# Optimization experiments

Measured on AMD Instinct MI355X. Metric: run time of the kernel, lower is better.

Reference implementation:

```python
import jax, jax.numpy as jnp
import numpy as np

N, E, FN, FE, L, G = 4096, 16384, 16, 8, 128, 64
EPS = 1e-5


def setup_inputs() -> dict:
    key = jax.random.key(0)
    ks = iter(jax.random.split(key, 40))

    def lin_w(shape):
        return jax.random.normal(next(ks), shape, jnp.float32) * (1.0 / np.sqrt(shape[0]))

    d = {}
    d["x"] = jax.random.normal(next(ks), (N, FN), jnp.float32)
    d["edge_attr"] = jax.random.normal(next(ks), (E, FE), jnp.float32)
    d["edge_index"] = jax.random.randint(next(ks), (2, E), 0, N)
    d["batch"] = jnp.sort(jax.random.randint(next(ks), (N,), 0, G))
    for i, (cin, cout) in enumerate([(FN, 32), (32, 64), (64, 128)], 1):
        d[f"We{i}"] = lin_w((FE, cin * cout))          # edge_fc weight
        d[f"be{i}"] = jnp.zeros((cin * cout,), jnp.float32)
        d[f"bias{i}"] = jnp.zeros((cout,), jnp.float32)
        d[f"Wr{i}"] = lin_w((cin, cout))               # res_fc weight
        d[f"br{i}"] = jnp.zeros((cout,), jnp.float32)
        d[f"bn_g{i}"] = jnp.ones((cout,), jnp.float32)
        d[f"bn_b{i}"] = jnp.zeros((cout,), jnp.float32)
        d[f"a{i}"] = jnp.float32(0.25)                  # PReLU slope
    d["Wi"] = lin_w((128, 128)); d["bi"] = jnp.zeros((128,), jnp.float32)
    d["Wj"] = lin_w((128, 128)); d["bj"] = jnp.zeros((128,), jnp.float32)
    d["Wfc"] = lin_w((128, 2 * L)); d["bfc"] = jnp.zeros((2 * L,), jnp.float32)
    return d


def _ecc(x, src, dst, norm, edge_attr, We, be, bias, Wr, br, cout, cin):
    # dynamically generated per-edge filter: [E, out, in]
    theta = (edge_attr @ We + be).reshape(E, cout, cin)
    # gather source features, per-edge matvec, degree-normalize (norm_j)
    msg = norm[src][:, None] * jnp.einsum('eoi,ei->eo', theta, x[src])
    # scatter-add into destination nodes + bias + residual linear
    return jax.ops.segment_sum(msg, dst, num_segments=N) + bias + x @ Wr + br


def _bn(x, g, b):
    m = x.mean(0)
    v = x.var(0)  # biased variance, as torch BN training normalization
    return (x - m) * jax.lax.rsqrt(v + EPS) * g + b


def _prelu(x, a):
    return jnp.where(x >= 0, x, a * x)


def reference(x, edge_attr, edge_index, batch,
              We1, be1, bias1, Wr1, br1, bn_g1, bn_b1, a1,
              We2, be2, bias2, Wr2, br2, bn_g2, bn_b2, a2,
              We3, be3, bias3, Wr3, br3, bn_g3, bn_b3, a3,
              Wi, bi, Wj, bj, Wfc, bfc):
    src, dst = edge_index[0], edge_index[1]
    deg = jax.ops.segment_sum(jnp.ones((E,), x.dtype), src, num_segments=N)
    norm = jnp.where(deg > 0, 1.0 / deg, 0.0)

    h = _ecc(x, src, dst, norm, edge_attr, We1, be1, bias1, Wr1, br1, 32, FN)
    h = _prelu(_bn(h, bn_g1, bn_b1), a1)
    h = _ecc(h, src, dst, norm, edge_attr, We2, be2, bias2, Wr2, br2, 64, 32)
    h = _prelu(_bn(h, bn_g2, bn_b2), a2)
    h = _ecc(h, src, dst, norm, edge_attr, We3, be3, bias3, Wr3, br3, 128, 64)
    h = _prelu(_bn(h, bn_g3, bn_b3), a3)

    # gated attention pooling (GGS-NN eq. 7), scatter-sum per graph
    gates = jax.nn.sigmoid(h @ Wi + bi)
    feats = jnp.tanh(h @ Wj + bj)
    pooled = jnp.tanh(jax.ops.segment_sum(gates * feats, batch, num_segments=G))

    z = pooled @ Wfc + bfc  # [G, 2L]
    return z[:, :L], z[:, L:]
```

## Files before the change

kernel.cpp:

```cpp
#include <hip/hip_runtime.h>
#include <math.h>

#define NN 4096
#define NE 16384
#define NG 64

#define OFF_DEG   0
#define OFF_H1    4096
#define OFF_H2    135168
#define OFF_H3    397312
#define OFF_ST1   921600
#define OFF_ST2   921664
#define OFF_ST3   921792
#define OFF_POOL  922048
#define OFF_WC1   930240
#define OFF_WC2   934848
#define OFF_WC3   953280
#define OFF_Y     1027008
#define ZERO_FLOATS 930240

__device__ __forceinline__ void tr_wcat(const float* We, const float* be,
                                        float* Wcat, int CIN, int COUT, int t) {
    int nine = 9 * COUT;
    int i = t / nine; int r = t - i * nine;
    int f = r / COUT; int o = r - f * COUT;
    Wcat[t] = (f < 8) ? We[f * CIN * COUT + o * CIN + i] : be[o * CIN + i];
}

__global__ __launch_bounds__(256) void k_prep(
    const float* __restrict__ We1, const float* __restrict__ be1,
    const float* __restrict__ We2, const float* __restrict__ be2,
    const float* __restrict__ We3, const float* __restrict__ be3,
    const int* __restrict__ ei, float* __restrict__ ws)
{
    int t = blockIdx.x * 256 + threadIdx.x;
    if (t < 4608)  { tr_wcat(We1, be1, ws + OFF_WC1, 16, 32, t); return; }
    t -= 4608;
    if (t < 18432) { tr_wcat(We2, be2, ws + OFF_WC2, 32, 64, t); return; }
    t -= 18432;
    if (t < 73728) { tr_wcat(We3, be3, ws + OFF_WC3, 64, 128, t); return; }
    t -= 73728;
    if (t < NE)    { atomicAdd(&ws[OFF_DEG + ei[t]], 1.0f); }
}

template<int K, bool BN>
__global__ __launch_bounds__(256) void k_proj(
    const float* __restrict__ A, const float* __restrict__ Bm,
    const float* __restrict__ deg, float* __restrict__ Y, int Ncols,
    const float* __restrict__ st, const float* __restrict__ g,
    const float* __restrict__ b, const float* __restrict__ a)
{
    __shared__ float sA[K][68];
    __shared__ float sB[K][68];
    __shared__ float sS[K];
    __shared__ float sT[K];
    const int tid = threadIdx.x;
    const int m0 = blockIdx.x * 64;
    const int n0 = blockIdx.y * 64;

    float al = 0.f;
    if constexpr (BN) {
        if (tid < K) {
            float mean = st[tid] * (1.f / NN);
            float var  = st[K + tid] * (1.f / NN) - mean * mean;
            var = fmaxf(var, 0.f);
            float s = rsqrtf(var + 1e-5f) * g[tid];
            sS[tid] = s;
            sT[tid] = b[tid] - mean * s;
        }
        al = a[0];
        __syncthreads();
    }

    for (int t = tid; t < 64 * K; t += 256) {
        int m = t / K, i = t - m * K;
        float v = A[(m0 + m) * K + i];
        if constexpr (BN) {
            v = fmaf(v, sS[i], sT[i]);
            v = v >= 0.f ? v : al * v;
        }
        sA[i][m] = v;
    }
    for (int t = tid; t < 64 * K; t += 256) {
        int i = t >> 6, n = t & 63;
        int col = n0 + n;
        sB[i][n] = (col < Ncols) ? Bm[i * Ncols + col] : 0.f;
    }
    __syncthreads();

    const int tn = tid & 15, tm = tid >> 4;
    float acc[4][4] = {{0.f}};
#pragma unroll 8
    for (int i = 0; i < K; ++i) {
        float4 av = *(const float4*)&sA[i][tm * 4];
        float4 bv = *(const float4*)&sB[i][tn * 4];
        acc[0][0] += av.x * bv.x; acc[0][1] += av.x * bv.y; acc[0][2] += av.x * bv.z; acc[0][3] += av.x * bv.w;
        acc[1][0] += av.y * bv.x; acc[1][1] += av.y * bv.y; acc[1][2] += av.y * bv.z; acc[1][3] += av.y * bv.w;
        acc[2][0] += av.z * bv.x; acc[2][1] += av.z * bv.y; acc[2][2] += av.z * bv.z; acc[2][3] += av.z * bv.w;
        acc[3][0] += av.w * bv.x; acc[3][1] += av.w * bv.y; acc[3][2] += av.w * bv.z; acc[3][3] += av.w * bv.w;
    }

#pragma unroll
    for (int mm = 0; mm < 4; ++mm) {
        int m = m0 + tm * 4 + mm;
        float d = deg[m];
        float nrm = d > 0.f ? 1.f / d : 0.f;
#pragma unroll
        for (int nn = 0; nn < 4; ++nn) {
            int col = n0 + tn * 4 + nn;
            if (col < Ncols) Y[(size_t)m * Ncols + col] = acc[mm][nn] * nrm;
        }
    }
}

template<int COUT>
__global__ __launch_bounds__(256) void k_egather(
    const float* __restrict__ Y, const float* __restrict__ eattr,
    const int* __restrict__ ei, float* __restrict__ h)
{
    int idx = blockIdx.x * 256 + threadIdx.x;
    int e = idx / COUT;
    int o = idx - e * COUT;
    int src = ei[e], dst = ei[NE + e];
    const float* y = Y + (size_t)src * (9 * COUT);
    const float* ea = eattr + e * 8;
    float acc = y[8 * COUT + o];
#pragma unroll
    for (int f = 0; f < 8; ++f) acc += ea[f] * y[f * COUT + o];
    atomicAdd(&h[dst * COUT + o], acc);
}

template<int CIN, int COUT, int KN, bool BN>
__global__ __launch_bounds__(256) void k_node(
    const float* __restrict__ xin, const float* __restrict__ Wr,
    const float* __restrict__ br, const float* __restrict__ bias,
    float* __restrict__ h, float* __restrict__ st_out,
    const float* __restrict__ st_in, const float* __restrict__ g,
    const float* __restrict__ b, const float* __restrict__ a)
{
    constexpr int NL = 256 / COUT;
    constexpr int NB = NL * KN;
    constexpr int CINP = CIN | 1;
    __shared__ float sWr[CIN * COUT];
    __shared__ float sX[NB * CINP];
    __shared__ float sred[256];
    __shared__ float sS[CIN];
    __shared__ float sT[CIN];
    const int tid = threadIdx.x;
    const int nbase = blockIdx.x * NB;

    if constexpr (BN) {
        if (tid < CIN) {
            float mean = st_in[tid] * (1.f / NN);
            float var  = st_in[CIN + tid] * (1.f / NN) - mean * mean;
            var = fmaxf(var, 0.f);
            float s = rsqrtf(var + 1e-5f) * g[tid];
            sS[tid] = s;
            sT[tid] = b[tid] - mean * s;
        }
    }
    for (int t = tid; t < CIN * COUT; t += 256) sWr[t] = Wr[t];
    __syncthreads();
    float al = 0.f;
    if constexpr (BN) al = a[0];

    for (int t = tid; t < NB * CIN; t += 256) {
        int r = t / CIN, i = t - r * CIN;
        float v = xin[(nbase + r) * CIN + i];
        if constexpr (BN) {
            v = fmaf(v, sS[i], sT[i]);
            v = v >= 0.f ? v : al * v;
        }
        sX[r * CINP + i] = v;
    }
    __syncthreads();

    const int o = tid % COUT;
    const int nl = tid / COUT;
    const float addc = bias[o] + br[o];
    float sum = 0.f, sumsq = 0.f;
#pragma unroll
    for (int k = 0; k < KN; ++k) {
        int r = nl * KN + k;
        float acc = addc;
        for (int i = 0; i < CIN; ++i)
            acc += sX[r * CINP + i] * sWr[i * COUT + o];
        int gi = (nbase + r) * COUT + o;
        float hv = h[gi] + acc;
        h[gi] = hv;
        sum += hv; sumsq += hv * hv;
    }
    sred[tid] = sum;
    __syncthreads();
    if (tid < COUT) {
        float s = 0.f;
        for (int q = 0; q < NL; ++q) s += sred[q * COUT + tid];
        atomicAdd(&st_out[tid], s);
    }
    __syncthreads();
    sred[tid] = sumsq;
    __syncthreads();
    if (tid < COUT) {
        float s = 0.f;
        for (int q = 0; q < NL; ++q) s += sred[q * COUT + tid];
        atomicAdd(&st_out[COUT + tid], s);
    }
}

__global__ __launch_bounds__(256) void k_pool(
    const float* __restrict__ h3, const int* __restrict__ batch,
    const float* __restrict__ Wi, const float* __restrict__ bi,
    const float* __restrict__ Wj, const float* __restrict__ bj,
    float* __restrict__ pooled,
    const float* __restrict__ st, const float* __restrict__ g,
    const float* __restrict__ b, const float* __restrict__ a)
{
    constexpr int KN = 8, NB = 16;
    __shared__ float sH[NB * 128];
    __shared__ int sB[NB];
    __shared__ float sS[128];
    __shared__ float sT[128];
    const int tid = threadIdx.x;
    const int nbase = blockIdx.x * NB;

    if (tid < 128) {
        float mean = st[tid] * (1.f / NN);
        float var  = st[128 + tid] * (1.f / NN) - mean * mean;
        var = fmaxf(var, 0.f);
        float s = rsqrtf(var + 1e-5f) * g[tid];
        sS[tid] = s;
        sT[tid] = b[tid] - mean * s;
    }
    if (tid < NB) sB[tid] = batch[nbase + tid];
    __syncthreads();
    const float al = a[0];

    for (int t = tid; t < NB * 128; t += 256) {
        int c = t & 127;
        float v = h3[nbase * 128 + t];
        v = fmaf(v, sS[c], sT[c]);
        v = v >= 0.f ? v : al * v;
        sH[t] = v;
    }
    __syncthreads();

    const int o = tid & 127, nl = tid >> 7;
    float gacc[KN], facc[KN];
#pragma unroll
    for (int k = 0; k < KN; ++k) { gacc[k] = 0.f; facc[k] = 0.f; }
    for (int i = 0; i < 128; ++i) {
        float wi = Wi[i * 128 + o], wj = Wj[i * 128 + o];
#pragma unroll
        for (int k = 0; k < KN; ++k) {
            float hv = sH[(nl * KN + k) * 128 + i];
            gacc[k] += hv * wi;
            facc[k] += hv * wj;
        }
    }
    float bio = bi[o], bjo = bj[o];
    float psum = 0.f;
    int curg = sB[nl * KN];
#pragma unroll
    for (int k = 0; k < KN; ++k) {
        int r = nl * KN + k;
        int bg = sB[r];
        if (bg != curg) {
            atomicAdd(&pooled[curg * 128 + o], psum);
            psum = 0.f; curg = bg;
        }
        float gate = 1.f / (1.f + expf(-(gacc[k] + bio)));
        float feat = tanhf(facc[k] + bjo);
        psum += gate * feat;
    }
    atomicAdd(&pooled[curg * 128 + o], psum);
}

__global__ __launch_bounds__(256) void k_final(
    const float* __restrict__ pooled, const float* __restrict__ Wfc,
    const float* __restrict__ bfc, float* __restrict__ out)
{
    __shared__ float sP[128];
    const int g = blockIdx.x, c = threadIdx.x;
    if (c < 128) sP[c] = tanhf(pooled[g * 128 + c]);
    __syncthreads();
    float z = bfc[c];
    for (int i = 0; i < 128; ++i) z += sP[i] * Wfc[i * 256 + c];
    int oidx = (c < 128) ? (g * 128 + c) : (NG * 128 + g * 128 + (c - 128));
    out[oidx] = z;
}

extern "C" void kernel_launch(void* const* d_in, const int* in_sizes, int n_in,
                              void* d_out, int out_size, void* d_ws, size_t ws_size,
                              hipStream_t stream)
{
    (void)in_sizes; (void)n_in; (void)out_size; (void)ws_size;
    const float* x     = (const float*)d_in[0];
    const float* eattr = (const float*)d_in[1];
    const int*   ei    = (const int*)d_in[2];
    const int*   batch = (const int*)d_in[3];
    const float* We1 = (const float*)d_in[4];
    const float* be1 = (const float*)d_in[5];
    const float* bias1 = (const float*)d_in[6];
    const float* Wr1 = (const float*)d_in[7];
    const float* br1 = (const float*)d_in[8];
    const float* bg1 = (const float*)d_in[9];
    const float* bb1 = (const float*)d_in[10];
    const float* a1  = (const float*)d_in[11];
    const float* We2 = (const float*)d_in[12];
    const float* be2 = (const float*)d_in[13];
    const float* bias2 = (const float*)d_in[14];
    const float* Wr2 = (const float*)d_in[15];
    const float* br2 = (const float*)d_in[16];
    const float* bg2 = (const float*)d_in[17];
    const float* bb2 = (const float*)d_in[18];
    const float* a2  = (const float*)d_in[19];
    const float* We3 = (const float*)d_in[20];
    const float* be3 = (const float*)d_in[21];
    const float* bias3 = (const float*)d_in[22];
    const float* Wr3 = (const float*)d_in[23];
    const float* br3 = (const float*)d_in[24];
    const float* bg3 = (const float*)d_in[25];
    const float* bb3 = (const float*)d_in[26];
    const float* a3  = (const float*)d_in[27];
    const float* Wi  = (const float*)d_in[28];
    const float* bi  = (const float*)d_in[29];
    const float* Wj  = (const float*)d_in[30];
    const float* bj  = (const float*)d_in[31];
    const float* Wfc = (const float*)d_in[32];
    const float* bfc = (const float*)d_in[33];
    float* ws  = (float*)d_ws;
    float* out = (float*)d_out;

    hipMemsetAsync(d_ws, 0, (size_t)ZERO_FLOATS * sizeof(float), stream);
    k_prep<<<442, 256, 0, stream>>>(We1, be1, We2, be2, We3, be3, ei, ws);

    k_proj<16, false><<<dim3(64, 5), 256, 0, stream>>>(
        x, ws + OFF_WC1, ws + OFF_DEG, ws + OFF_Y, 288,
        nullptr, nullptr, nullptr, nullptr);
    k_egather<32><<<NE * 32 / 256, 256, 0, stream>>>(ws + OFF_Y, eattr, ei, ws + OFF_H1);
    k_node<16, 32, 2, false><<<NN / 16, 256, 0, stream>>>(
        x, Wr1, br1, bias1, ws + OFF_H1, ws + OFF_ST1,
        nullptr, nullptr, nullptr, nullptr);

    k_proj<32, true><<<dim3(64, 9), 256, 0, stream>>>(
        ws + OFF_H1, ws + OFF_WC2, ws + OFF_DEG, ws + OFF_Y, 576,
        ws + OFF_ST1, bg1, bb1, a1);
    k_egather<64><<<NE * 64 / 256, 256, 0, stream>>>(ws + OFF_Y, eattr, ei, ws + OFF_H2);
    k_node<32, 64, 4, true><<<NN / 16, 256, 0, stream>>>(
        ws + OFF_H1, Wr2, br2, bias2, ws + OFF_H2, ws + OFF_ST2,
        ws + OFF_ST1, bg1, bb1, a1);

    k_proj<64, true><<<dim3(64, 18), 256, 0, stream>>>(
        ws + OFF_H2, ws + OFF_WC3, ws + OFF_DEG, ws + OFF_Y, 1152,
        ws + OFF_ST2, bg2, bb2, a2);
    k_egather<128><<<NE * 128 / 256, 256, 0, stream>>>(ws + OFF_Y, eattr, ei, ws + OFF_H3);
    k_node<64, 128, 8, true><<<NN / 16, 256, 0, stream>>>(
        ws + OFF_H2, Wr3, br3, bias3, ws + OFF_H3, ws + OFF_ST3,
        ws + OFF_ST2, bg2, bb2, a2);

    k_pool<<<NN / 16, 256, 0, stream>>>(ws + OFF_H3, batch, Wi, bi, Wj, bj, ws + OFF_POOL,
                                        ws + OFF_ST3, bg3, bb3, a3);
    k_final<<<NG, 256, 0, stream>>>(ws + OFF_POOL, Wfc, bfc, out);
}
```

Before: 261.0 us.

## Fuse residual linear and weight transpose into projection GEMM, move degree norm to gather

The projection GEMM now reads the edge-filter weights directly in transposed form and appends the residual linear (Wr) as extra output columns. It writes h as the residual plus biases, so the edge-gather atomics accumulate on top of it. The separate prep kernel is removed: the degree count runs as extra blocks of the first projection, and degree normalization moves into the edge gather. The node kernel shrinks to a statistics-only pass, which cuts launches and the memset size. The risk is a race on the degree array: it is counted in the same launch as the first projection, and the gather reads it afterwards, so ordering holds. The uncoalesced transposed weight reads inside each GEMM block are an added cost.

```diff
diff --git a/kernel.cpp b/kernel.cpp
--- a/kernel.cpp
+++ b/kernel.cpp
@@ -6,57 +6,49 @@
 #define NG 64
 
 #define OFF_DEG   0
-#define OFF_H1    4096
-#define OFF_H2    135168
-#define OFF_H3    397312
-#define OFF_ST1   921600
-#define OFF_ST2   921664
-#define OFF_ST3   921792
-#define OFF_POOL  922048
-#define OFF_WC1   930240
-#define OFF_WC2   934848
-#define OFF_WC3   953280
-#define OFF_Y     1027008
-#define ZERO_FLOATS 930240
-
-__device__ __forceinline__ void tr_wcat(const float* We, const float* be,
-                                        float* Wcat, int CIN, int COUT, int t) {
-    int nine = 9 * COUT;
-    int i = t / nine; int r = t - i * nine;
-    int f = r / COUT; int o = r - f * COUT;
-    Wcat[t] = (f < 8) ? We[f * CIN * COUT + o * CIN + i] : be[o * CIN + i];
-}
-
-__global__ __launch_bounds__(256) void k_prep(
-    const float* __restrict__ We1, const float* __restrict__ be1,
-    const float* __restrict__ We2, const float* __restrict__ be2,
-    const float* __restrict__ We3, const float* __restrict__ be3,
-    const int* __restrict__ ei, float* __restrict__ ws)
-{
-    int t = blockIdx.x * 256 + threadIdx.x;
-    if (t < 4608)  { tr_wcat(We1, be1, ws + OFF_WC1, 16, 32, t); return; }
-    t -= 4608;
-    if (t < 18432) { tr_wcat(We2, be2, ws + OFF_WC2, 32, 64, t); return; }
-    t -= 18432;
-    if (t < 73728) { tr_wcat(We3, be3, ws + OFF_WC3, 64, 128, t); return; }
-    t -= 73728;
-    if (t < NE)    { atomicAdd(&ws[OFF_DEG + ei[t]], 1.0f); }
-}
-
-template<int K, bool BN>
+#define OFF_ST1   4096
+#define OFF_ST2   4160
+#define OFF_ST3   4288
+#define OFF_POOL  4544
+#define ZERO_FLOATS 12736
+#define OFF_H1    12736
+#define OFF_H2    143808
+#define OFF_H3    405952
+#define OFF_Y     930240
+
+template<int K, int COUT, bool BN, bool DEG>
 __global__ __launch_bounds__(256) void k_proj(
-    const float* __restrict__ A, const float* __restrict__ Bm,
-    const float* __restrict__ deg, float* __restrict__ Y, int Ncols,
+    const float* __restrict__ A,
+    const float* __restrict__ We, const float* __restrict__ be,
+    const float* __restrict__ Wr, const float* __restrict__ bias,
+    const float* __restrict__ br,
+    const int* __restrict__ ei, float* __restrict__ deg,
+    float* __restrict__ Y, float* __restrict__ h,
     const float* __restrict__ st, const float* __restrict__ g,
     const float* __restrict__ b, const float* __restrict__ a)
 {
+    constexpr int NCOL = 10 * COUT;
+    constexpr int NY = NCOL / 64;
+    constexpr int NC9 = 9 * COUT;
+    constexpr int L2C = (COUT == 32) ? 5 : (COUT == 64) ? 6 : 7;
+
+    const int tid = threadIdx.x;
+    const int bid = blockIdx.x;
+
+    if constexpr (DEG) {
+        if (bid >= 64 * NY) {
+            int e = (bid - 64 * NY) * 256 + tid;
+            if (e < NE) atomicAdd(&deg[ei[e]], 1.0f);
+            return;
+        }
+    }
+
     __shared__ float sA[K][68];
     __shared__ float sB[K][68];
     __shared__ float sS[K];
     __shared__ float sT[K];
-    const int tid = threadIdx.x;
-    const int m0 = blockIdx.x * 64;
-    const int n0 = blockIdx.y * 64;
+    const int m0 = (bid & 63) * 64;
+    const int n0 = (bid >> 6) * 64;
 
     float al = 0.f;
     if constexpr (BN) {
@@ -84,7 +76,13 @@
     for (int t = tid; t < 64 * K; t += 256) {
         int i = t >> 6, n = t & 63;
         int col = n0 + n;
-        sB[i][n] = (col < Ncols) ? Bm[i * Ncols + col] : 0.f;
+        int f = col >> L2C;
+        int o = col & (COUT - 1);
+        float v;
+        if (f < 8)       v = We[f * K * COUT + o * K + i];
+        else if (f == 8) v = be[o * K + i];
+        else             v = Wr[i * COUT + o];
+        sB[i][n] = v;
     }
     __syncthreads();
 
@@ -103,12 +101,15 @@
 #pragma unroll
     for (int mm = 0; mm < 4; ++mm) {
         int m = m0 + tm * 4 + mm;
-        float d = deg[m];
-        float nrm = d > 0.f ? 1.f / d : 0.f;
 #pragma unroll
         for (int nn = 0; nn < 4; ++nn) {
             int col = n0 + tn * 4 + nn;
-            if (col < Ncols) Y[(size_t)m * Ncols + col] = acc[mm][nn] * nrm;
+            if (col < NC9) {
+                Y[(size_t)m * NC9 + col] = acc[mm][nn];
+            } else {
+                int o = col - NC9;
+                h[m * COUT + o] = acc[mm][nn] + bias[o] + br[o];
+            }
         }
     }
 }
@@ -116,86 +117,48 @@
 template<int COUT>
 __global__ __launch_bounds__(256) void k_egather(
     const float* __restrict__ Y, const float* __restrict__ eattr,
-    const int* __restrict__ ei, float* __restrict__ h)
+    const int* __restrict__ ei, const float* __restrict__ deg,
+    float* __restrict__ h)
 {
     int idx = blockIdx.x * 256 + threadIdx.x;
     int e = idx / COUT;
     int o = idx - e * COUT;
     int src = ei[e], dst = ei[NE + e];
+    float d = deg[src];
+    float nrm = d > 0.f ? 1.f / d : 0.f;
     const float* y = Y + (size_t)src * (9 * COUT);
     const float* ea = eattr + e * 8;
     float acc = y[8 * COUT + o];
 #pragma unroll
     for (int f = 0; f < 8; ++f) acc += ea[f] * y[f * COUT + o];
-    atomicAdd(&h[dst * COUT + o], acc);
-}
-
-template<int CIN, int COUT, int KN, bool BN>
-__global__ __launch_bounds__(256) void k_node(
-    const float* __restrict__ xin, const float* __restrict__ Wr,
-    const float* __restrict__ br, const float* __restrict__ bias,
-    float* __restrict__ h, float* __restrict__ st_out,
-    const float* __restrict__ st_in, const float* __restrict__ g,
-    const float* __restrict__ b, const float* __restrict__ a)
+    atomicAdd(&h[dst * COUT + o], nrm * acc);
+}
+
+template<int COUT>
+__global__ __launch_bounds__(256) void k_stats(
+    const float* __restrict__ h, float* __restrict__ st)
 {
     constexpr int NL = 256 / COUT;
-    constexpr int NB = NL * KN;
-    constexpr int CINP = CIN | 1;
-    __shared__ float sWr[CIN * COUT];
-    __shared__ float sX[NB * CINP];
+    constexpr int KN = 16 / NL;
     __shared__ float sred[256];
-    __shared__ float sS[CIN];
-    __shared__ float sT[CIN];
     const int tid = threadIdx.x;
-    const int nbase = blockIdx.x * NB;
-
-    if constexpr (BN) {
-        if (tid < CIN) {
-            float mean = st_in[tid] * (1.f / NN);
-            float var  = st_in[CIN + tid] * (1.f / NN) - mean * mean;
-            var = fmaxf(var, 0.f);
-            float s = rsqrtf(var + 1e-5f) * g[tid];
-            sS[tid] = s;
-            sT[tid] = b[tid] - mean * s;
-        }
-    }
-    for (int t = tid; t < CIN * COUT; t += 256) sWr[t] = Wr[t];
-    __syncthreads();
-    float al = 0.f;
-    if constexpr (BN) al = a[0];
-
-    for (int t = tid; t < NB * CIN; t += 256) {
-        int r = t / CIN, i = t - r * CIN;
-        float v = xin[(nbase + r) * CIN + i];
-        if constexpr (BN) {
-            v = fmaf(v, sS[i], sT[i]);
-            v = v >= 0.f ? v : al * v;
-        }
-        sX[r * CINP + i] = v;
-    }
-    __syncthreads();
-
+    const int nbase = blockIdx.x * 16;
     const int o = tid % COUT;
     const int nl = tid / COUT;
-    const float addc = bias[o] + br[o];
+
     float sum = 0.f, sumsq = 0.f;
 #pragma unroll
     for (int k = 0; k < KN; ++k) {
         int r = nl * KN + k;
-        float acc = addc;
-        for (int i = 0; i < CIN; ++i)
-            acc += sX[r * CINP + i] * sWr[i * COUT + o];
-        int gi = (nbase + r) * COUT + o;
-        float hv = h[gi] + acc;
-        h[gi] = hv;
-        sum += hv; sumsq += hv * hv;
+        float v = h[(nbase + r) * COUT + o];
+        sum += v; sumsq += v * v;
     }
     sred[tid] = sum;
     __syncthreads();
     if (tid < COUT) {
         float s = 0.f;
         for (int q = 0; q < NL; ++q) s += sred[q * COUT + tid];
-        atomicAdd(&st_out[tid], s);
+        atomicAdd(&st[tid], s);
     }
     __syncthreads();
     sred[tid] = sumsq;
@@ -203,7 +166,7 @@
     if (tid < COUT) {
         float s = 0.f;
         for (int q = 0; q < NL; ++q) s += sred[q * COUT + tid];
-        atomicAdd(&st_out[COUT + tid], s);
+        atomicAdd(&st[COUT + tid], s);
     }
 }
 
@@ -332,31 +295,27 @@
     float* out = (float*)d_out;
 
     hipMemsetAsync(d_ws, 0, (size_t)ZERO_FLOATS * sizeof(float), stream);
-    k_prep<<<442, 256, 0, stream>>>(We1, be1, We2, be2, We3, be3, ei, ws);
-
-    k_proj<16, false><<<dim3(64, 5), 256, 0, stream>>>(
-        x, ws + OFF_WC1, ws + OFF_DEG, ws + OFF_Y, 288,
-        nullptr, nullptr, nullptr, nullptr);
-    k_egather<32><<<NE * 32 / 256, 256, 0, stream>>>(ws + OFF_Y, eattr, ei, ws + OFF_H1);
-    k_node<16, 32, 2, false><<<NN / 16, 256, 0, stream>>>(
-        x, Wr1, br1, bias1, ws + OFF_H1, ws + OFF_ST1,
-        nullptr, nullptr, nullptr, nullptr);
-
-    k_proj<32, true><<<dim3(64, 9), 256, 0, stream>>>(
-        ws + OFF_H1, ws + OFF_WC2, ws + OFF_DEG, ws + OFF_Y, 576,
-        ws + OFF_ST1, bg1, bb1, a1);
-    k_egather<64><<<NE * 64 / 256, 256, 0, stream>>>(ws + OFF_Y, eattr, ei, ws + OFF_H2);
-    k_node<32, 64, 4, true><<<NN / 16, 256, 0, stream>>>(
-        ws + OFF_H1, Wr2, br2, bias2, ws + OFF_H2, ws + OFF_ST2,
-        ws + OFF_ST1, bg1, bb1, a1);
-
-    k_proj<64, true><<<dim3(64, 18), 256, 0, stream>>>(
-        ws + OFF_H2, ws + OFF_WC3, ws + OFF_DEG, ws + OFF_Y, 1152,
-        ws + OFF_ST2, bg2, bb2, a2);
-    k_egather<128><<<NE * 128 / 256, 256, 0, stream>>>(ws + OFF_Y, eattr, ei, ws + OFF_H3);
-    k_node<64, 128, 8, true><<<NN / 16, 256, 0, stream>>>(
-        ws + OFF_H2, Wr3, br3, bias3, ws + OFF_H3, ws + OFF_ST3,
-        ws + OFF_ST2, bg2, bb2, a2);
+
+    k_proj<16, 32, false, true><<<64 * 5 + 64, 256, 0, stream>>>(
+        x, We1, be1, Wr1, bias1, br1, ei, ws + OFF_DEG,
+        ws + OFF_Y, ws + OFF_H1, nullptr, nullptr, nullptr, nullptr);
+    k_egather<32><<<NE * 32 / 256, 256, 0, stream>>>(
+        ws + OFF_Y, eattr, ei, ws + OFF_DEG, ws + OFF_H1);
+    k_stats<32><<<NN / 16, 256, 0, stream>>>(ws + OFF_H1, ws + OFF_ST1);
+
+    k_proj<32, 64, true, false><<<64 * 10, 256, 0, stream>>>(
+        ws + OFF_H1, We2, be2, Wr2, bias2, br2, nullptr, nullptr,
+        ws + OFF_Y, ws + OFF_H2, ws + OFF_ST1, bg1, bb1, a1);
+    k_egather<64><<<NE * 64 / 256, 256, 0, stream>>>(
+        ws + OFF_Y, eattr, ei, ws + OFF_DEG, ws + OFF_H2);
+    k_stats<64><<<NN / 16, 256, 0, stream>>>(ws + OFF_H2, ws + OFF_ST2);
+
+    k_proj<64, 128, true, false><<<64 * 20, 256, 0, stream>>>(
+        ws + OFF_H2, We3, be3, Wr3, bias3, br3, nullptr, nullptr,
+        ws + OFF_Y, ws + OFF_H3, ws + OFF_ST2, bg2, bb2, a2);
+    k_egather<128><<<NE * 128 / 256, 256, 0, stream>>>(
+        ws + OFF_Y, eattr, ei, ws + OFF_DEG, ws + OFF_H3);
+    k_stats<128><<<NN / 16, 256, 0, stream>>>(ws + OFF_H3, ws + OFF_ST3);
 
     k_pool<<<NN / 16, 256, 0, stream>>>(ws + OFF_H3, batch, Wi, bi, Wj, bj, ws + OFF_POOL,
                                         ws + OFF_ST3, bg3, bb3, a3);
```

New measurement: 240.5 us (median of 2 runs). 7.9% less time.
